# Optimization experiments

Measured on AMD Instinct MI355X. Metric: run time of the kernel, lower is better.

The kernel has to match this reference:

```python
import jax, jax.numpy as jnp
import numpy as np

B, S, E, D, A = 64, 1024, 512, 512, 512

def setup_inputs() -> dict:
    key = jax.random.key(0)
    ks = jax.random.split(key, 12)
    xavier = lambda k, shape: jax.random.uniform(k, shape, jnp.float32,
        -jnp.sqrt(6.0 / (shape[0] + shape[1])), jnp.sqrt(6.0 / (shape[0] + shape[1])))
    return {
        "encoder_states": jax.random.normal(ks[0], (B, S, E), jnp.float32),
        "decoder_state": jax.random.normal(ks[1], (B, D), jnp.float32),
        "encoder_mask": jnp.ones((B, S), jnp.int32),
        "coverage": jax.random.uniform(ks[2], (B, S), jnp.float32),
        # learned parameters (torch nn.Linear: y = x @ W.T + b)
        "W_enc": xavier(ks[3], (A, E)),           # encoder_projection, no bias
        "W_dec": xavier(ks[4], (A, D)),           # decoder_projection, no bias
        "w_attn": xavier(ks[5], (1, A)),          # attention_weight, no bias
        "W_layer1": xavier(ks[6], (A, A)),        # attention_layers[0]
        "b_layer1": jnp.zeros((A,), jnp.float32),
        "W_cov": xavier(ks[7], (A, 1)),           # coverage_projection, no bias
        "W_gate": xavier(ks[8], (A, E + D)),      # gate Linear
        "b_gate": jnp.zeros((A,), jnp.float32),
    }


def reference(encoder_states, decoder_state, encoder_mask, coverage,
              W_enc, W_dec, w_attn, W_layer1, b_layer1, W_cov, W_gate, b_gate):
    # projections
    proj_enc = jnp.einsum('bse,ae->bsa', encoder_states, W_enc)        # [B,S,A]
    proj_dec = jnp.einsum('bd,ad->ba', decoder_state, W_dec)[:, None]  # [B,1,A]
    attn_in = proj_enc + proj_dec
    # coverage: Linear(1->A) on coverage[..., None]
    attn_in = attn_in + coverage[..., None] * W_cov[None, None, :, 0]  # [B,S,A]
    feats = jnp.tanh(attn_in)
    # extra residual tanh layer (num_layers=2 -> one layer)
    feats = jnp.tanh(jnp.einsum('bsa,ca->bsc', feats, W_layer1) + b_layer1 + feats)
    scores = jnp.einsum('bsa,a->bs', feats, w_attn[0])                 # [B,S]
    scores = jnp.where(encoder_mask == 0, -1e9, scores)
    attn_w = jax.nn.softmax(scores, axis=-1)                           # [B,S]
    context = jnp.einsum('bs,bse->be', attn_w, encoder_states)         # [B,E]
    # gating
    gate_in = jnp.concatenate([context, decoder_state], axis=-1)       # [B,E+D]
    gate = jax.nn.sigmoid(jnp.einsum('bf,af->ba', gate_in, W_gate) + b_gate)
    context = gate * context
    updated_coverage = coverage + attn_w
    return (context, attn_w, updated_coverage)
```

## Files before the change

kernel.cpp:

```cpp
#include <hip/hip_runtime.h>
#include <hip/hip_bf16.h>

typedef unsigned short ushort_t;
typedef __attribute__((ext_vector_type(8))) short short8;
typedef __attribute__((ext_vector_type(4))) float float4_t;
typedef __attribute__((ext_vector_type(2))) float float2_t;
typedef __attribute__((ext_vector_type(4))) unsigned int uint4_t;

#define BB 64
#define SS 1024
#define EE 512
#define DD 512
#define AA 512
#define MM (BB*SS)
#define KK 512
#define BM 128
#define BN 128
#define BK 32
#define BKP 40
#define BK2 64
#define NT (KK/BK2)

__device__ __forceinline__ float bf2f(ushort_t u) {
    return __uint_as_float(((unsigned int)u) << 16);
}
__device__ __forceinline__ ushort_t f2bf(float f) {
    unsigned int u = __float_as_uint(f);
    unsigned int r = u + 0x7fffu + ((u >> 16) & 1u);
    return (ushort_t)(r >> 16);
}
__device__ __forceinline__ float ldmix(int f32, const void* p, long idx) {
    return f32 ? ((const float*)p)[idx] : bf2f(((const ushort_t*)p)[idx]);
}
__device__ __forceinline__ void stmix(int f32, void* p, long idx, float v) {
    if (f32) ((float*)p)[idx] = v;
    else     ((ushort_t*)p)[idx] = f2bf(v);
}
__device__ __forceinline__ float fast_tanh(float x) {
    float e = __expf(2.f * x);
    return 1.f - 2.f / (e + 1.f);
}
__device__ __forceinline__ void glds16(const ushort_t* g, ushort_t* l) {
    typedef __attribute__((address_space(1))) const void gas_t;
    typedef __attribute__((address_space(3))) void las_t;
    gas_t* gp = (gas_t*)g;
    las_t* lp = (las_t*)l;
    __builtin_amdgcn_global_load_lds(gp, lp, 16, 0, 0);
}

__global__ void k_detect(const ushort_t* __restrict__ enc, int* __restrict__ flag) {
    __shared__ int cnt;
    int tid = threadIdx.x;
    if (tid == 0) cnt = 0;
    __syncthreads();
    int c = 0;
    const uint4_t* p = (const uint4_t*)enc;
    for (int i = tid; i < 4096; i += 256) {
        uint4_t v = p[i];
        #pragma unroll
        for (int j = 0; j < 4; j++) {
            unsigned int u = v[j];
            if (((u >> 7) & 0xFFu) == 0xFFu || ((u >> 23) & 0xFFu) == 0xFFu) c++;
        }
    }
    atomicAdd(&cnt, c);
    __syncthreads();
    if (tid == 0) *flag = (cnt > 0) ? 1 : 0;
}

__global__ __launch_bounds__(256)
void k_conv_w(const void* __restrict__ Wenc, const void* __restrict__ W1,
              const int* __restrict__ flagp,
              ushort_t* __restrict__ WencB, ushort_t* __restrict__ W1B) {
    const int f32 = *flagp;
    const void* src = blockIdx.y ? W1 : Wenc;
    ushort_t* dst = blockIdx.y ? W1B : WencB;
    long e0 = ((long)blockIdx.x * 256 + threadIdx.x) * 8;
    short8 p;
    #pragma unroll
    for (int j = 0; j < 8; j++) p[j] = (short)f2bf(ldmix(f32, src, e0 + j));
    *(short8*)&dst[e0] = p;
}

__global__ __launch_bounds__(256)
void k_conv_enc(const void* __restrict__ enc, const int* __restrict__ flagp,
                ushort_t* __restrict__ out) {
    if (*flagp == 0) return;
    const float4_t* src = (const float4_t*)enc;
    size_t i0 = (size_t)blockIdx.x * 256 + threadIdx.x;
    size_t n8 = (size_t)MM * EE / 8;
    size_t stride = (size_t)gridDim.x * 256;
    for (size_t i = i0; i < n8; i += stride) {
        float4_t v0 = src[2 * i], v1 = src[2 * i + 1];
        short8 p;
        p[0] = (short)f2bf(v0[0]); p[1] = (short)f2bf(v0[1]);
        p[2] = (short)f2bf(v0[2]); p[3] = (short)f2bf(v0[3]);
        p[4] = (short)f2bf(v1[0]); p[5] = (short)f2bf(v1[1]);
        p[6] = (short)f2bf(v1[2]); p[7] = (short)f2bf(v1[3]);
        *(short8*)&out[i * 8] = p;
    }
}

__global__ __launch_bounds__(256)
void k_proj_dec(const void* __restrict__ dec,
                const void* __restrict__ Wdec,
                const int* __restrict__ flagp,
                float* __restrict__ proj) {
    __shared__ float x[DD];
    const int f32 = *flagp;
    const int b = blockIdx.y;
    const int tid = threadIdx.x, lane = tid & 63, wave = tid >> 6;
    x[tid]       = ldmix(f32, dec, (long)b * DD + tid);
    x[tid + 256] = ldmix(f32, dec, (long)b * DD + tid + 256);
    __syncthreads();
    const int a = blockIdx.x * 4 + wave;
    float s = 0.f;
    if (f32) {
        const float* wr = (const float*)Wdec + (size_t)a * DD + lane * 8;
        #pragma unroll
        for (int j = 0; j < 8; j++) s += wr[j] * x[lane * 8 + j];
    } else {
        const ushort_t* wr = (const ushort_t*)Wdec + (size_t)a * DD + lane * 8;
        short8 w = *(const short8*)wr;
        #pragma unroll
        for (int j = 0; j < 8; j++) s += bf2f((ushort_t)w[j]) * x[lane * 8 + j];
    }
    #pragma unroll
    for (int off = 1; off < 64; off <<= 1) s += __shfl_xor(s, off);
    if (lane == 0) proj[b * AA + a] = s;
}

__device__ __forceinline__ void stage8(int f32, const void* g, long row, int col,
                                       ushort_t* lds) {
    if (f32) {
        const float* gf = (const float*)g + row * KK + col;
        float4_t v0 = *(const float4_t*)(gf);
        float4_t v1 = *(const float4_t*)(gf + 4);
        short8 p;
        p[0] = (short)f2bf(v0[0]); p[1] = (short)f2bf(v0[1]);
        p[2] = (short)f2bf(v0[2]); p[3] = (short)f2bf(v0[3]);
        p[4] = (short)f2bf(v1[0]); p[5] = (short)f2bf(v1[1]);
        p[6] = (short)f2bf(v1[2]); p[7] = (short)f2bf(v1[3]);
        *(short8*)lds = p;
    } else {
        const ushort_t* gb = (const ushort_t*)g + row * KK + col;
        *(short8*)lds = *(const short8*)gb;
    }
}

__global__ __launch_bounds__(256)
void k_gemm1(const void* __restrict__ Xg,
             const void* __restrict__ Bg,
             const float* __restrict__ proj_dec,
             const void* __restrict__ cov,
             const void* __restrict__ Wcov,
             const int* __restrict__ flagp,
             ushort_t* __restrict__ feats) {
    __shared__ ushort_t As[BM * BKP];
    __shared__ ushort_t Bs[BN * BKP];
    const int f32 = *flagp;
    const int tid = threadIdx.x;
    const int lane = tid & 63, wave = tid >> 6;
    const int quad = lane >> 4, l16 = lane & 15;
    const int wm = wave >> 1, wn = wave & 1;
    const int m0 = blockIdx.y * BM, n0 = blockIdx.x * BN;

    float4_t acc[4][4];
    #pragma unroll
    for (int i = 0; i < 4; i++)
        #pragma unroll
        for (int j = 0; j < 4; j++) acc[i][j] = (float4_t){0.f, 0.f, 0.f, 0.f};

    const int srow = lane >> 2;
    const int scol = (lane & 3) * 8;
    ushort_t* lA0 = &As[(wave * 32 + srow) * BKP + scol];
    ushort_t* lB0 = &Bs[(wave * 32 + srow) * BKP + scol];

    for (int kt = 0; kt < KK; kt += BK) {
        __syncthreads();
        stage8(f32, Xg, (long)(m0 + wave * 32 + srow), kt + scol, lA0);
        stage8(f32, Xg, (long)(m0 + wave * 32 + srow + 16), kt + scol, lA0 + 16 * BKP);
        stage8(f32, Bg, (long)(n0 + wave * 32 + srow), kt + scol, lB0);
        stage8(f32, Bg, (long)(n0 + wave * 32 + srow + 16), kt + scol, lB0 + 16 * BKP);
        __syncthreads();
        short8 af[4], bfr[4];
        #pragma unroll
        for (int mt = 0; mt < 4; mt++)
            af[mt] = *(const short8*)&As[(wm * 64 + mt * 16 + l16) * BKP + quad * 8];
        #pragma unroll
        for (int nt = 0; nt < 4; nt++)
            bfr[nt] = *(const short8*)&Bs[(wn * 64 + nt * 16 + l16) * BKP + quad * 8];
        #pragma unroll
        for (int mt = 0; mt < 4; mt++)
            #pragma unroll
            for (int nt = 0; nt < 4; nt++)
                acc[mt][nt] = __builtin_amdgcn_mfma_f32_16x16x32_bf16(af[mt], bfr[nt], acc[mt][nt], 0, 0, 0);
    }

    #pragma unroll
    for (int mt = 0; mt < 4; mt++) {
        #pragma unroll
        for (int r = 0; r < 4; r++) {
            int m = m0 + wm * 64 + mt * 16 + quad * 4 + r;
            int b = m >> 10;
            float covv = ldmix(f32, cov, m);
            #pragma unroll
            for (int nt = 0; nt < 4; nt++) {
                int n = n0 + wn * 64 + nt * 16 + l16;
                float v = acc[mt][nt][r] + proj_dec[b * AA + n] + covv * ldmix(f32, Wcov, n);
                feats[(size_t)m * AA + n] = f2bf(fast_tanh(v));
            }
        }
    }
}

__global__ __launch_bounds__(256)
void k_gemm2(const ushort_t* __restrict__ Xg,
             const void* __restrict__ Bg,
             const void* __restrict__ b1,
             const void* __restrict__ wattn,
             const int* __restrict__ flagp,
             float* __restrict__ scores) {
    __shared__ ushort_t As[BM * BKP];
    __shared__ ushort_t Bs[BN * BKP];
    const int f32 = *flagp;
    const int tid = threadIdx.x;
    const int lane = tid & 63, wave = tid >> 6;
    const int quad = lane >> 4, l16 = lane & 15;
    const int wm = wave >> 1, wn = wave & 1;
    const int m0 = blockIdx.y * BM, n0 = blockIdx.x * BN;

    float4_t acc[4][4];
    #pragma unroll
    for (int i = 0; i < 4; i++)
        #pragma unroll
        for (int j = 0; j < 4; j++) acc[i][j] = (float4_t){0.f, 0.f, 0.f, 0.f};

    const int srow = lane >> 2;
    const int scol = (lane & 3) * 8;
    ushort_t* lA0 = &As[(wave * 32 + srow) * BKP + scol];
    ushort_t* lB0 = &Bs[(wave * 32 + srow) * BKP + scol];

    for (int kt = 0; kt < KK; kt += BK) {
        __syncthreads();
        stage8(0,   Xg, (long)(m0 + wave * 32 + srow), kt + scol, lA0);
        stage8(0,   Xg, (long)(m0 + wave * 32 + srow + 16), kt + scol, lA0 + 16 * BKP);
        stage8(f32, Bg, (long)(n0 + wave * 32 + srow), kt + scol, lB0);
        stage8(f32, Bg, (long)(n0 + wave * 32 + srow + 16), kt + scol, lB0 + 16 * BKP);
        __syncthreads();
        short8 af[4], bfr[4];
        #pragma unroll
        for (int mt = 0; mt < 4; mt++)
            af[mt] = *(const short8*)&As[(wm * 64 + mt * 16 + l16) * BKP + quad * 8];
        #pragma unroll
        for (int nt = 0; nt < 4; nt++)
            bfr[nt] = *(const short8*)&Bs[(wn * 64 + nt * 16 + l16) * BKP + quad * 8];
        #pragma unroll
        for (int mt = 0; mt < 4; mt++)
            #pragma unroll
            for (int nt = 0; nt < 4; nt++)
                acc[mt][nt] = __builtin_amdgcn_mfma_f32_16x16x32_bf16(af[mt], bfr[nt], acc[mt][nt], 0, 0, 0);
    }

    float wv[4], bv[4];
    #pragma unroll
    for (int nt = 0; nt < 4; nt++) {
        int n = n0 + wn * 64 + nt * 16 + l16;
        wv[nt] = ldmix(f32, wattn, n);
        bv[nt] = ldmix(f32, b1, n);
    }
    #pragma unroll
    for (int mt = 0; mt < 4; mt++) {
        #pragma unroll
        for (int r = 0; r < 4; r++) {
            int m = m0 + wm * 64 + mt * 16 + quad * 4 + r;
            float s = 0.f;
            #pragma unroll
            for (int nt = 0; nt < 4; nt++) {
                int n = n0 + wn * 64 + nt * 16 + l16;
                float v = acc[mt][nt][r] + bv[nt] + bf2f(Xg[(size_t)m * AA + n]);
                s += fast_tanh(v) * wv[nt];
            }
            s += __shfl_xor(s, 1);
            s += __shfl_xor(s, 2);
            s += __shfl_xor(s, 4);
            s += __shfl_xor(s, 8);
            if (l16 == 0) atomicAdd(&scores[m], s);
        }
    }
}

__global__ __launch_bounds__(256)
void k_gemm1n(const void* __restrict__ enc,
              const ushort_t* __restrict__ enc_bf,
              const ushort_t* __restrict__ Wenc_bf,
              const float* __restrict__ proj_dec,
              const void* __restrict__ cov,
              const void* __restrict__ Wcov,
              const int* __restrict__ flagp,
              ushort_t* __restrict__ feats) {
    __shared__ ushort_t As[BM * BK2];
    __shared__ ushort_t Bs[BN * BK2];
    const int f32 = *flagp;
    const ushort_t* Abf = f32 ? enc_bf : (const ushort_t*)enc;

    const int lid = ((blockIdx.x & 7) << 8) | (blockIdx.x >> 3);
    const int m0 = (lid >> 2) * BM;
    const int n0 = (lid & 3) * BN;

    const int tid = threadIdx.x;
    const int lane = tid & 63, wave = tid >> 6;
    const int quad = lane >> 4, l16 = lane & 15;
    const int wm = wave >> 1, wn = wave & 1;
    const int l8r = lane >> 3;
    const int l8c = ((lane & 7) ^ l8r) * 8;

    float4_t acc[4][4];
    #pragma unroll
    for (int i = 0; i < 4; i++)
        #pragma unroll
        for (int j = 0; j < 4; j++) acc[i][j] = (float4_t){0.f, 0.f, 0.f, 0.f};

    #pragma unroll
    for (int kt = 0; kt < NT; kt++) {
        __syncthreads();
        #pragma unroll
        for (int i = 0; i < 4; i++) {
            int ch = i * 4 + wave;
            glds16(Abf     + (((size_t)(m0 + ch * 8 + l8r)) << 9) + kt * BK2 + l8c, &As[ch * 512]);
            glds16(Wenc_bf + (((size_t)(n0 + ch * 8 + l8r)) << 9) + kt * BK2 + l8c, &Bs[ch * 512]);
        }
        __syncthreads();
        #pragma unroll
        for (int kk = 0; kk < 2; kk++) {
            short8 af[4], bfv[4];
            #pragma unroll
            for (int mt = 0; mt < 4; mt++) {
                int row = wm * 64 + mt * 16 + l16;
                int col = (kk * 32 + quad * 8) ^ ((row & 7) << 3);
                af[mt] = *(const short8*)&As[row * BK2 + col];
            }
            #pragma unroll
            for (int nt = 0; nt < 4; nt++) {
                int row = wn * 64 + nt * 16 + l16;
                int col = (kk * 32 + quad * 8) ^ ((row & 7) << 3);
                bfv[nt] = *(const short8*)&Bs[row * BK2 + col];
            }
            #pragma unroll
            for (int mt = 0; mt < 4; mt++)
                #pragma unroll
                for (int nt = 0; nt < 4; nt++)
                    acc[mt][nt] = __builtin_amdgcn_mfma_f32_16x16x32_bf16(af[mt], bfv[nt], acc[mt][nt], 0, 0, 0);
        }
    }

    __syncthreads();
    ushort_t* myhalf = wm ? Bs : As;
    #pragma unroll
    for (int mt = 0; mt < 4; mt++) {
        #pragma unroll
        for (int r = 0; r < 4; r++) {
            int lr = mt * 16 + quad * 4 + r;
            int grow = wm * 64 + lr;
            int m = m0 + grow;
            int b = m >> 10;
            float covv = ldmix(f32, cov, m);
            #pragma unroll
            for (int nt = 0; nt < 4; nt++) {
                int lc = wn * 64 + nt * 16 + l16;
                int n = n0 + lc;
                float v = acc[mt][nt][r] + proj_dec[b * AA + n] + covv * ldmix(f32, Wcov, n);
                myhalf[lr * 128 + (lc ^ ((grow & 7) << 3))] = f2bf(fast_tanh(v));
            }
        }
    }
    __syncthreads();
    #pragma unroll
    for (int rep = 0; rep < 8; rep++) {
        int row = rep * 16 + (tid >> 4);
        int c8 = (tid & 15) * 8;
        const ushort_t* half = (row < 64) ? As : Bs;
        short8 vv = *(const short8*)&half[(row & 63) * 128 + (c8 ^ ((row & 7) << 3))];
        *(short8*)&feats[(size_t)(m0 + row) * AA + n0 + c8] = vv;
    }
}

__global__ __launch_bounds__(256)
void k_gemm2n(const ushort_t* __restrict__ Xg,
              const ushort_t* __restrict__ W1_bf,
              const void* __restrict__ b1,
              const void* __restrict__ wattn,
              const int* __restrict__ flagp,
              float* __restrict__ scores) {
    __shared__ ushort_t As[BM * BK2];
    __shared__ ushort_t Bs[BN * BK2];
    const int f32 = *flagp;

    const int lid = ((blockIdx.x & 7) << 8) | (blockIdx.x >> 3);
    const int m0 = (lid >> 2) * BM;
    const int n0 = (lid & 3) * BN;

    const int tid = threadIdx.x;
    const int lane = tid & 63, wave = tid >> 6;
    const int quad = lane >> 4, l16 = lane & 15;
    const int wm = wave >> 1, wn = wave & 1;
    const int l8r = lane >> 3;
    const int l8c = ((lane & 7) ^ l8r) * 8;

    float4_t acc[4][4];
    #pragma unroll
    for (int i = 0; i < 4; i++)
        #pragma unroll
        for (int j = 0; j < 4; j++) acc[i][j] = (float4_t){0.f, 0.f, 0.f, 0.f};

    #pragma unroll
    for (int kt = 0; kt < NT; kt++) {
        __syncthreads();
        #pragma unroll
        for (int i = 0; i < 4; i++) {
            int ch = i * 4 + wave;
            glds16(Xg    + (((size_t)(m0 + ch * 8 + l8r)) << 9) + kt * BK2 + l8c, &As[ch * 512]);
            glds16(W1_bf + (((size_t)(n0 + ch * 8 + l8r)) << 9) + kt * BK2 + l8c, &Bs[ch * 512]);
        }
        __syncthreads();
        #pragma unroll
        for (int kk = 0; kk < 2; kk++) {
            short8 af[4], bfv[4];
            #pragma unroll
            for (int mt = 0; mt < 4; mt++) {
                int row = wm * 64 + mt * 16 + l16;
                int col = (kk * 32 + quad * 8) ^ ((row & 7) << 3);
                af[mt] = *(const short8*)&As[row * BK2 + col];
            }
            #pragma unroll
            for (int nt = 0; nt < 4; nt++) {
                int row = wn * 64 + nt * 16 + l16;
                int col = (kk * 32 + quad * 8) ^ ((row & 7) << 3);
                bfv[nt] = *(const short8*)&Bs[row * BK2 + col];
            }
            #pragma unroll
            for (int mt = 0; mt < 4; mt++)
                #pragma unroll
                for (int nt = 0; nt < 4; nt++)
                    acc[mt][nt] = __builtin_amdgcn_mfma_f32_16x16x32_bf16(af[mt], bfv[nt], acc[mt][nt], 0, 0, 0);
        }
    }

    float wv[4], bv[4];
    #pragma unroll
    for (int nt = 0; nt < 4; nt++) {
        int n = n0 + wn * 64 + nt * 16 + l16;
        wv[nt] = ldmix(f32, wattn, n);
        bv[nt] = ldmix(f32, b1, n);
    }
    #pragma unroll
    for (int mt = 0; mt < 4; mt++) {
        #pragma unroll
        for (int r = 0; r < 4; r++) {
            int m = m0 + wm * 64 + mt * 16 + quad * 4 + r;
            float s = 0.f;
            #pragma unroll
            for (int nt = 0; nt < 4; nt++) {
                int n = n0 + wn * 64 + nt * 16 + l16;
                float v = acc[mt][nt][r] + bv[nt] + bf2f(Xg[(size_t)m * AA + n]);
                s += fast_tanh(v) * wv[nt];
            }
            s += __shfl_xor(s, 1);
            s += __shfl_xor(s, 2);
            s += __shfl_xor(s, 4);
            s += __shfl_xor(s, 8);
            if (l16 == 0) atomicAdd(&scores[m], s);
        }
    }
}

__global__ void k_softmax(const float* __restrict__ scores,
                          const int* __restrict__ mask,
                          const void* __restrict__ cov,
                          const int* __restrict__ flagp,
                          float* __restrict__ attnw,
                          void* __restrict__ dout) {
    __shared__ float red[4];
    const int f32 = *flagp;
    int b = blockIdx.x, tid = threadIdx.x;
    float v[4];
    #pragma unroll
    for (int i = 0; i < 4; i++) {
        int s = tid + i * 256;
        float sc = scores[b * SS + s];
        if (mask[b * SS + s] == 0) sc = -1e9f;
        v[i] = sc;
    }
    float mx = fmaxf(fmaxf(v[0], v[1]), fmaxf(v[2], v[3]));
    #pragma unroll
    for (int off = 1; off < 64; off <<= 1) mx = fmaxf(mx, __shfl_xor(mx, off));
    if ((tid & 63) == 0) red[tid >> 6] = mx;
    __syncthreads();
    mx = fmaxf(fmaxf(red[0], red[1]), fmaxf(red[2], red[3]));
    __syncthreads();
    float e[4], sum = 0.f;
    #pragma unroll
    for (int i = 0; i < 4; i++) { e[i] = expf(v[i] - mx); sum += e[i]; }
    #pragma unroll
    for (int off = 1; off < 64; off <<= 1) sum += __shfl_xor(sum, off);
    if ((tid & 63) == 0) red[tid >> 6] = sum;
    __syncthreads();
    sum = red[0] + red[1] + red[2] + red[3];
    float inv = 1.0f / sum;
    #pragma unroll
    for (int i = 0; i < 4; i++) {
        int s = tid + i * 256;
        float w = e[i] * inv;
        attnw[b * SS + s] = w;
        stmix(f32, dout, 32768L + (long)b * SS + s, w);
        stmix(f32, dout, 98304L + (long)b * SS + s, ldmix(f32, cov, (long)b * SS + s) + w);
    }
}

__global__ void k_context_p(const void* __restrict__ enc,
                            const ushort_t* __restrict__ enc_bf,
                            const float* __restrict__ attnw,
                            const int* __restrict__ flagp,
                            float2_t* __restrict__ ctxp) {
    const int f32 = *flagp;
    const unsigned int* base = (const unsigned int*)(f32 ? (const void*)enc_bf : enc);
    int b = blockIdx.x, sc = blockIdx.y;
    int tid = threadIdx.x;
    base += ((size_t)b * SS + sc * 128) * (EE / 2);
    float a0 = 0.f, a1 = 0.f;
    const float* wrow = attnw + b * SS + sc * 128;
    for (int s = 0; s < 128; s++) {
        float w = wrow[s];
        unsigned int u = base[(size_t)s * (EE / 2) + tid];
        a0 += w * bf2f((ushort_t)(u & 0xffff));
        a1 += w * bf2f((ushort_t)(u >> 16));
    }
    ctxp[((b << 3) + sc) * 256 + tid] = (float2_t){a0, a1};
}

__global__ void k_context(const void* __restrict__ enc,
                          const ushort_t* __restrict__ enc_bf,
                          const int pre,
                          const float* __restrict__ attnw,
                          const int* __restrict__ flagp,
                          float* __restrict__ ctx) {
    int f32 = *flagp;
    const void* e = enc;
    if (pre && f32) { e = enc_bf; f32 = 0; }
    int b = blockIdx.x, sc = blockIdx.y;
    int tid = threadIdx.x;
    float a0 = 0.f, a1 = 0.f;
    const float* wrow = attnw + b * SS + sc * 128;
    if (f32) {
        const float* base = (const float*)e + ((size_t)b * SS + sc * 128) * EE;
        for (int s = 0; s < 128; s++) {
            float w = wrow[s];
            float2_t u = *(const float2_t*)(base + (size_t)s * EE + 2 * tid);
            a0 += w * u[0];
            a1 += w * u[1];
        }
    } else {
        const unsigned int* base = (const unsigned int*)e + ((size_t)b * SS + sc * 128) * (EE / 2);
        for (int s = 0; s < 128; s++) {
            float w = wrow[s];
            unsigned int u = base[(size_t)s * (EE / 2) + tid];
            a0 += w * bf2f((ushort_t)(u & 0xffff));
            a1 += w * bf2f((ushort_t)(u >> 16));
        }
    }
    atomicAdd(&ctx[b * EE + 2 * tid], a0);
    atomicAdd(&ctx[b * EE + 2 * tid + 1], a1);
}

__global__ __launch_bounds__(256)
void k_gate_p(const float2_t* __restrict__ ctxp,
              const void* __restrict__ dec,
              const void* __restrict__ Wg,
              const void* __restrict__ bg,
              const int* __restrict__ flagp,
              void* __restrict__ dout) {
    __shared__ float gin[EE + DD];
    const int f32 = *flagp;
    const int b = blockIdx.y;
    const int tid = threadIdx.x, lane = tid & 63, wave = tid >> 6;
    float c0 = 0.f, c1 = 0.f;
    #pragma unroll
    for (int sc = 0; sc < 8; sc++) {
        float2_t v = ctxp[((b << 3) + sc) * 256 + tid];
        c0 += v[0]; c1 += v[1];
    }
    gin[2 * tid] = c0;
    gin[2 * tid + 1] = c1;
    gin[EE + tid]       = ldmix(f32, dec, (long)b * DD + tid);
    gin[EE + tid + 256] = ldmix(f32, dec, (long)b * DD + tid + 256);
    __syncthreads();
    const int a = blockIdx.x * 4 + wave;
    float s = 0.f;
    if (f32) {
        const float* wr = (const float*)Wg + (size_t)a * (EE + DD) + lane * 16;
        #pragma unroll
        for (int j = 0; j < 16; j++) s += wr[j] * gin[lane * 16 + j];
    } else {
        const ushort_t* wr = (const ushort_t*)Wg + (size_t)a * (EE + DD) + lane * 16;
        short8 w0 = *(const short8*)wr;
        short8 w1 = *(const short8*)(wr + 8);
        #pragma unroll
        for (int j = 0; j < 8; j++) {
            s += bf2f((ushort_t)w0[j]) * gin[lane * 16 + j];
            s += bf2f((ushort_t)w1[j]) * gin[lane * 16 + 8 + j];
        }
    }
    #pragma unroll
    for (int off = 1; off < 64; off <<= 1) s += __shfl_xor(s, off);
    if (lane == 0) {
        float acc = s + ldmix(f32, bg, a);
        float g = 1.f / (1.f + __expf(-acc));
        stmix(f32, dout, (long)b * AA + a, g * gin[a]);
    }
}

__global__ __launch_bounds__(256)
void k_gate(const float* __restrict__ ctx,
            const void* __restrict__ dec,
            const void* __restrict__ Wg,
            const void* __restrict__ bg,
            const int* __restrict__ flagp,
            void* __restrict__ dout) {
    __shared__ float gin[EE + DD];
    const int f32 = *flagp;
    const int b = blockIdx.y;
    const int tid = threadIdx.x, lane = tid & 63, wave = tid >> 6;
    gin[2 * tid]     = ctx[b * EE + 2 * tid];
    gin[2 * tid + 1] = ctx[b * EE + 2 * tid + 1];
    gin[EE + tid]       = ldmix(f32, dec, (long)b * DD + tid);
    gin[EE + tid + 256] = ldmix(f32, dec, (long)b * DD + tid + 256);
    __syncthreads();
    const int a = blockIdx.x * 4 + wave;
    float s = 0.f;
    if (f32) {
        const float* wr = (const float*)Wg + (size_t)a * (EE + DD) + lane * 16;
        #pragma unroll
        for (int j = 0; j < 16; j++) s += wr[j] * gin[lane * 16 + j];
    } else {
        const ushort_t* wr = (const ushort_t*)Wg + (size_t)a * (EE + DD) + lane * 16;
        short8 w0 = *(const short8*)wr;
        short8 w1 = *(const short8*)(wr + 8);
        #pragma unroll
        for (int j = 0; j < 8; j++) {
            s += bf2f((ushort_t)w0[j]) * gin[lane * 16 + j];
            s += bf2f((ushort_t)w1[j]) * gin[lane * 16 + 8 + j];
        }
    }
    #pragma unroll
    for (int off = 1; off < 64; off <<= 1) s += __shfl_xor(s, off);
    if (lane == 0) {
        float acc = s + ldmix(f32, bg, a);
        float g = 1.f / (1.f + __expf(-acc));
        stmix(f32, dout, (long)b * AA + a, g * ctx[b * EE + a]);
    }
}

extern "C" void kernel_launch(void* const* d_in, const int* in_sizes, int n_in,
                              void* d_out, int out_size, void* d_ws, size_t ws_size,
                              hipStream_t stream) {
    const void* enc   = d_in[0];
    const void* dec   = d_in[1];
    const int*  mask  = (const int*)d_in[2];
    const void* cov   = d_in[3];
    const void* Wenc  = d_in[4];
    const void* Wdec  = d_in[5];
    const void* wattn = d_in[6];
    const void* Wl1   = d_in[7];
    const void* b1    = d_in[8];
    const void* Wcov  = d_in[9];
    const void* Wg    = d_in[10];
    const void* bg    = d_in[11];

    char* ws = (char*)d_ws;
    float*    scores = (float*)ws;
    float*    ctx    = (float*)(ws + 262144);
    float*    attnw  = (float*)(ws + 393216);
    float*    projd  = (float*)(ws + 655360);
    int*      flag   = (int*)(ws + 786432);
    ushort_t* feats  = (ushort_t*)(ws + 1048576);
    ushort_t* W1b    = (ushort_t*)(ws + 68157440);
    ushort_t* Wencb  = (ushort_t*)(ws + 68681728);
    ushort_t* encb   = (ushort_t*)(ws + 69206016);
    float2_t* ctxp   = (float2_t*)(ws + 136314880);
    const int pre2 = (ws_size >= 69206016UL)  ? 1 : 0;
    const int pre1 = (ws_size >= 136314880UL) ? 1 : 0;
    const int pre3 = (ws_size >= 137363456UL) ? 1 : 0;

    hipMemsetAsync(ws, 0, 393216, stream);
    k_detect<<<1, 256, 0, stream>>>((const ushort_t*)enc, flag);
    if (pre2)
        k_conv_w<<<dim3(128, 2), 256, 0, stream>>>(Wenc, Wl1, flag, Wencb, W1b);
    if (pre1)
        k_conv_enc<<<4096, 256, 0, stream>>>(enc, flag, encb);
    k_proj_dec<<<dim3(AA / 4, BB), 256, 0, stream>>>(dec, Wdec, flag, projd);
    if (pre1)
        k_gemm1n<<<2048, 256, 0, stream>>>(enc, encb, Wencb, projd, cov, Wcov, flag, feats);
    else
        k_gemm1<<<dim3(AA / BN, MM / BM), 256, 0, stream>>>(enc, Wenc, projd, cov, Wcov, flag, feats);
    if (pre2)
        k_gemm2n<<<2048, 256, 0, stream>>>(feats, W1b, b1, wattn, flag, scores);
    else
        k_gemm2<<<dim3(AA / BN, MM / BM), 256, 0, stream>>>(feats, Wl1, b1, wattn, flag, scores);
    k_softmax<<<BB, 256, 0, stream>>>(scores, mask, cov, flag, attnw, d_out);
    if (pre1 && pre3) {
        k_context_p<<<dim3(BB, 8), 256, 0, stream>>>(enc, encb, attnw, flag, ctxp);
        k_gate_p<<<dim3(AA / 4, BB), 256, 0, stream>>>(ctxp, dec, Wg, bg, flag, d_out);
    } else {
        k_context<<<dim3(BB, 8), 256, 0, stream>>>(enc, encb, pre1, attnw, flag, ctx);
        k_gate<<<dim3(AA / 4, BB), 256, 0, stream>>>(ctx, dec, Wg, bg, flag, d_out);
    }
}
```

Baseline: 399.6 us.

## Fuse prep kernels, write per-slice partial scores, infer dtype from input sizes

Merges encoder/weight bf16 conversion and decoder projection into a single prep launch. The score GEMM now writes per-column-block partial sums to separate slots, which the softmax adds up, so the atomic/memset path is no longer needed. The dtype is taken from host-side input sizes, which skips the detect kernel when the size is recognized. The new path needs a larger workspace and costs extra partial-score traffic.

```diff
diff --git a/kernel.cpp b/kernel.cpp
--- a/kernel.cpp
+++ b/kernel.cpp
@@ -40,6 +40,9 @@
     float e = __expf(2.f * x);
     return 1.f - 2.f / (e + 1.f);
 }
+__device__ __forceinline__ int getf32(const int* flagp, int fmode) {
+    return (fmode == 2) ? *flagp : fmode;
+}
 __device__ __forceinline__ void glds16(const ushort_t* g, ushort_t* l) {
     typedef __attribute__((address_space(1))) const void gas_t;
     typedef __attribute__((address_space(3))) void las_t;
@@ -69,10 +72,71 @@
 }
 
 __global__ __launch_bounds__(256)
+void k_prep(const void* __restrict__ enc, const void* __restrict__ dec,
+            const void* __restrict__ Wenc, const void* __restrict__ W1,
+            const void* __restrict__ Wdec, const int* __restrict__ flagp, const int fmode,
+            ushort_t* __restrict__ encb, ushort_t* __restrict__ WencB,
+            ushort_t* __restrict__ W1B, float* __restrict__ proj) {
+    __shared__ float x[DD];
+    const int f32 = getf32(flagp, fmode);
+    const int bx = blockIdx.x, tid = threadIdx.x;
+    if (bx < 4096) {
+        if (!f32) return;
+        const float4_t* src = (const float4_t*)enc;
+        size_t i0 = (size_t)bx * 256 + tid;
+        size_t n8 = (size_t)MM * EE / 8;
+        size_t stride = (size_t)4096 * 256;
+        for (size_t i = i0; i < n8; i += stride) {
+            float4_t v0 = src[2 * i], v1 = src[2 * i + 1];
+            short8 p;
+            p[0] = (short)f2bf(v0[0]); p[1] = (short)f2bf(v0[1]);
+            p[2] = (short)f2bf(v0[2]); p[3] = (short)f2bf(v0[3]);
+            p[4] = (short)f2bf(v1[0]); p[5] = (short)f2bf(v1[1]);
+            p[6] = (short)f2bf(v1[2]); p[7] = (short)f2bf(v1[3]);
+            *(short8*)&encb[i * 8] = p;
+        }
+        return;
+    }
+    if (bx < 4352) {
+        int idx = bx - 4096;
+        int by = idx >> 7, bxx = idx & 127;
+        const void* src = by ? W1 : Wenc;
+        ushort_t* dst = by ? W1B : WencB;
+        long e0 = ((long)bxx * 256 + tid) * 8;
+        short8 p;
+        #pragma unroll
+        for (int j = 0; j < 8; j++) p[j] = (short)f2bf(ldmix(f32, src, e0 + j));
+        *(short8*)&dst[e0] = p;
+        return;
+    }
+    int q = bx - 4352;
+    const int bxx = q & 127, b = q >> 7;
+    const int lane = tid & 63, wave = tid >> 6;
+    x[tid]       = ldmix(f32, dec, (long)b * DD + tid);
+    x[tid + 256] = ldmix(f32, dec, (long)b * DD + tid + 256);
+    __syncthreads();
+    const int a = bxx * 4 + wave;
+    float s = 0.f;
+    if (f32) {
+        const float* wr = (const float*)Wdec + (size_t)a * DD + lane * 8;
+        #pragma unroll
+        for (int j = 0; j < 8; j++) s += wr[j] * x[lane * 8 + j];
+    } else {
+        const ushort_t* wr = (const ushort_t*)Wdec + (size_t)a * DD + lane * 8;
+        short8 w = *(const short8*)wr;
+        #pragma unroll
+        for (int j = 0; j < 8; j++) s += bf2f((ushort_t)w[j]) * x[lane * 8 + j];
+    }
+    #pragma unroll
+    for (int off = 1; off < 64; off <<= 1) s += __shfl_xor(s, off);
+    if (lane == 0) proj[b * AA + a] = s;
+}
+
+__global__ __launch_bounds__(256)
 void k_conv_w(const void* __restrict__ Wenc, const void* __restrict__ W1,
-              const int* __restrict__ flagp,
+              const int* __restrict__ flagp, const int fmode,
               ushort_t* __restrict__ WencB, ushort_t* __restrict__ W1B) {
-    const int f32 = *flagp;
+    const int f32 = getf32(flagp, fmode);
     const void* src = blockIdx.y ? W1 : Wenc;
     ushort_t* dst = blockIdx.y ? W1B : WencB;
     long e0 = ((long)blockIdx.x * 256 + threadIdx.x) * 8;
@@ -83,9 +147,9 @@
 }
 
 __global__ __launch_bounds__(256)
-void k_conv_enc(const void* __restrict__ enc, const int* __restrict__ flagp,
+void k_conv_enc(const void* __restrict__ enc, const int* __restrict__ flagp, const int fmode,
                 ushort_t* __restrict__ out) {
-    if (*flagp == 0) return;
+    if (getf32(flagp, fmode) == 0) return;
     const float4_t* src = (const float4_t*)enc;
     size_t i0 = (size_t)blockIdx.x * 256 + threadIdx.x;
     size_t n8 = (size_t)MM * EE / 8;
@@ -104,10 +168,10 @@
 __global__ __launch_bounds__(256)
 void k_proj_dec(const void* __restrict__ dec,
                 const void* __restrict__ Wdec,
-                const int* __restrict__ flagp,
+                const int* __restrict__ flagp, const int fmode,
                 float* __restrict__ proj) {
     __shared__ float x[DD];
-    const int f32 = *flagp;
+    const int f32 = getf32(flagp, fmode);
     const int b = blockIdx.y;
     const int tid = threadIdx.x, lane = tid & 63, wave = tid >> 6;
     x[tid]       = ldmix(f32, dec, (long)b * DD + tid);
@@ -154,11 +218,11 @@
              const float* __restrict__ proj_dec,
              const void* __restrict__ cov,
              const void* __restrict__ Wcov,
-             const int* __restrict__ flagp,
+             const int* __restrict__ flagp, const int fmode,
              ushort_t* __restrict__ feats) {
     __shared__ ushort_t As[BM * BKP];
     __shared__ ushort_t Bs[BN * BKP];
-    const int f32 = *flagp;
+    const int f32 = getf32(flagp, fmode);
     const int tid = threadIdx.x;
     const int lane = tid & 63, wave = tid >> 6;
     const int quad = lane >> 4, l16 = lane & 15;
@@ -219,11 +283,11 @@
              const void* __restrict__ Bg,
              const void* __restrict__ b1,
              const void* __restrict__ wattn,
-             const int* __restrict__ flagp,
+             const int* __restrict__ flagp, const int fmode,
              float* __restrict__ scores) {
     __shared__ ushort_t As[BM * BKP];
     __shared__ ushort_t Bs[BN * BKP];
-    const int f32 = *flagp;
+    const int f32 = getf32(flagp, fmode);
     const int tid = threadIdx.x;
     const int lane = tid & 63, wave = tid >> 6;
     const int quad = lane >> 4, l16 = lane & 15;
@@ -297,11 +361,11 @@
               const float* __restrict__ proj_dec,
               const void* __restrict__ cov,
               const void* __restrict__ Wcov,
-              const int* __restrict__ flagp,
+              const int* __restrict__ flagp, const int fmode,
               ushort_t* __restrict__ feats) {
     __shared__ ushort_t As[BM * BK2];
     __shared__ ushort_t Bs[BN * BK2];
-    const int f32 = *flagp;
+    const int f32 = getf32(flagp, fmode);
     const ushort_t* Abf = f32 ? enc_bf : (const ushort_t*)enc;
 
     const int lid = ((blockIdx.x & 7) << 8) | (blockIdx.x >> 3);
@@ -386,19 +450,20 @@
 }
 
 __global__ __launch_bounds__(256)
-void k_gemm2n(const ushort_t* __restrict__ Xg,
+void k_gemm2p(const ushort_t* __restrict__ Xg,
               const ushort_t* __restrict__ W1_bf,
               const void* __restrict__ b1,
               const void* __restrict__ wattn,
-              const int* __restrict__ flagp,
-              float* __restrict__ scores) {
+              const int* __restrict__ flagp, const int fmode,
+              float* __restrict__ sp) {
     __shared__ ushort_t As[BM * BK2];
     __shared__ ushort_t Bs[BN * BK2];
-    const int f32 = *flagp;
+    const int f32 = getf32(flagp, fmode);
 
     const int lid = ((blockIdx.x & 7) << 8) | (blockIdx.x >> 3);
     const int m0 = (lid >> 2) * BM;
     const int n0 = (lid & 3) * BN;
+    const int nb = lid & 3;
 
     const int tid = threadIdx.x;
     const int lane = tid & 63, wave = tid >> 6;
@@ -453,6 +518,96 @@
         wv[nt] = ldmix(f32, wattn, n);
         bv[nt] = ldmix(f32, b1, n);
     }
+    const size_t slotbase = (size_t)(nb * 2 + wn) * MM;
+    #pragma unroll
+    for (int mt = 0; mt < 4; mt++) {
+        #pragma unroll
+        for (int r = 0; r < 4; r++) {
+            int m = m0 + wm * 64 + mt * 16 + quad * 4 + r;
+            float s = 0.f;
+            #pragma unroll
+            for (int nt = 0; nt < 4; nt++) {
+                int n = n0 + wn * 64 + nt * 16 + l16;
+                float v = acc[mt][nt][r] + bv[nt] + bf2f(Xg[(size_t)m * AA + n]);
+                s += fast_tanh(v) * wv[nt];
+            }
+            s += __shfl_xor(s, 1);
+            s += __shfl_xor(s, 2);
+            s += __shfl_xor(s, 4);
+            s += __shfl_xor(s, 8);
+            if (l16 == 0) sp[slotbase + m] = s;
+        }
+    }
+}
+
+__global__ __launch_bounds__(256)
+void k_gemm2n(const ushort_t* __restrict__ Xg,
+              const ushort_t* __restrict__ W1_bf,
+              const void* __restrict__ b1,
+              const void* __restrict__ wattn,
+              const int* __restrict__ flagp, const int fmode,
+              float* __restrict__ scores) {
+    __shared__ ushort_t As[BM * BK2];
+    __shared__ ushort_t Bs[BN * BK2];
+    const int f32 = getf32(flagp, fmode);
+
+    const int lid = ((blockIdx.x & 7) << 8) | (blockIdx.x >> 3);
+    const int m0 = (lid >> 2) * BM;
+    const int n0 = (lid & 3) * BN;
+
+    const int tid = threadIdx.x;
+    const int lane = tid & 63, wave = tid >> 6;
+    const int quad = lane >> 4, l16 = lane & 15;
+    const int wm = wave >> 1, wn = wave & 1;
+    const int l8r = lane >> 3;
+    const int l8c = ((lane & 7) ^ l8r) * 8;
+
+    float4_t acc[4][4];
+    #pragma unroll
+    for (int i = 0; i < 4; i++)
+        #pragma unroll
+        for (int j = 0; j < 4; j++) acc[i][j] = (float4_t){0.f, 0.f, 0.f, 0.f};
+
+    #pragma unroll
+    for (int kt = 0; kt < NT; kt++) {
+        __syncthreads();
+        #pragma unroll
+        for (int i = 0; i < 4; i++) {
+            int ch = i * 4 + wave;
+            glds16(Xg    + (((size_t)(m0 + ch * 8 + l8r)) << 9) + kt * BK2 + l8c, &As[ch * 512]);
+            glds16(W1_bf + (((size_t)(n0 + ch * 8 + l8r)) << 9) + kt * BK2 + l8c, &Bs[ch * 512]);
+        }
+        __syncthreads();
+        #pragma unroll
+        for (int kk = 0; kk < 2; kk++) {
+            short8 af[4], bfv[4];
+            #pragma unroll
+            for (int mt = 0; mt < 4; mt++) {
+                int row = wm * 64 + mt * 16 + l16;
+                int col = (kk * 32 + quad * 8) ^ ((row & 7) << 3);
+                af[mt] = *(const short8*)&As[row * BK2 + col];
+            }
+            #pragma unroll
+            for (int nt = 0; nt < 4; nt++) {
+                int row = wn * 64 + nt * 16 + l16;
+                int col = (kk * 32 + quad * 8) ^ ((row & 7) << 3);
+                bfv[nt] = *(const short8*)&Bs[row * BK2 + col];
+            }
+            #pragma unroll
+            for (int mt = 0; mt < 4; mt++)
+                #pragma unroll
+                for (int nt = 0; nt < 4; nt++)
+                    acc[mt][nt] = __builtin_amdgcn_mfma_f32_16x16x32_bf16(af[mt], bfv[nt], acc[mt][nt], 0, 0, 0);
+        }
+    }
+
+    float wv[4], bv[4];
+    #pragma unroll
+    for (int nt = 0; nt < 4; nt++) {
+        int n = n0 + wn * 64 + nt * 16 + l16;
+        wv[nt] = ldmix(f32, wattn, n);
+        bv[nt] = ldmix(f32, b1, n);
+    }
     #pragma unroll
     for (int mt = 0; mt < 4; mt++) {
         #pragma unroll
@@ -474,20 +629,22 @@
     }
 }
 
-__global__ void k_softmax(const float* __restrict__ scores,
-                          const int* __restrict__ mask,
-                          const void* __restrict__ cov,
-                          const int* __restrict__ flagp,
-                          float* __restrict__ attnw,
-                          void* __restrict__ dout) {
+__global__ void k_softmax_p(const float* __restrict__ sp,
+                            const int* __restrict__ mask,
+                            const void* __restrict__ cov,
+                            const int* __restrict__ flagp, const int fmode,
+                            float* __restrict__ attnw,
+                            void* __restrict__ dout) {
     __shared__ float red[4];
-    const int f32 = *flagp;
+    const int f32 = getf32(flagp, fmode);
     int b = blockIdx.x, tid = threadIdx.x;
     float v[4];
     #pragma unroll
     for (int i = 0; i < 4; i++) {
         int s = tid + i * 256;
-        float sc = scores[b * SS + s];
+        float sc = 0.f;
+        #pragma unroll
+        for (int k = 0; k < 8; k++) sc += sp[(size_t)k * MM + b * SS + s];
         if (mask[b * SS + s] == 0) sc = -1e9f;
         v[i] = sc;
     }
@@ -517,12 +674,55 @@
     }
 }
 
+__global__ void k_softmax(const float* __restrict__ scores,
+                          const int* __restrict__ mask,
+                          const void* __restrict__ cov,
+                          const int* __restrict__ flagp, const int fmode,
+                          float* __restrict__ attnw,
+                          void* __restrict__ dout) {
+    __shared__ float red[4];
+    const int f32 = getf32(flagp, fmode);
+    int b = blockIdx.x, tid = threadIdx.x;
+    float v[4];
+    #pragma unroll
+    for (int i = 0; i < 4; i++) {
+        int s = tid + i * 256;
+        float sc = scores[b * SS + s];
+        if (mask[b * SS + s] == 0) sc = -1e9f;
+        v[i] = sc;
+    }
+    float mx = fmaxf(fmaxf(v[0], v[1]), fmaxf(v[2], v[3]));
+    #pragma unroll
+    for (int off = 1; off < 64; off <<= 1) mx = fmaxf(mx, __shfl_xor(mx, off));
+    if ((tid & 63) == 0) red[tid >> 6] = mx;
+    __syncthreads();
+    mx = fmaxf(fmaxf(red[0], red[1]), fmaxf(red[2], red[3]));
+    __syncthreads();
+    float e[4], sum = 0.f;
+    #pragma unroll
+    for (int i = 0; i < 4; i++) { e[i] = expf(v[i] - mx); sum += e[i]; }
+    #pragma unroll
+    for (int off = 1; off < 64; off <<= 1) sum += __shfl_xor(sum, off);
+    if ((tid & 63) == 0) red[tid >> 6] = sum;
+    __syncthreads();
+    sum = red[0] + red[1] + red[2] + red[3];
+    float inv = 1.0f / sum;
+    #pragma unroll
+    for (int i = 0; i < 4; i++) {
+        int s = tid + i * 256;
+        float w = e[i] * inv;
+        attnw[b * SS + s] = w;
+        stmix(f32, dout, 32768L + (long)b * SS + s, w);
+        stmix(f32, dout, 98304L + (long)b * SS + s, ldmix(f32, cov, (long)b * SS + s) + w);
+    }
+}
+
 __global__ void k_context_p(const void* __restrict__ enc,
                             const ushort_t* __restrict__ enc_bf,
                             const float* __restrict__ attnw,
-                            const int* __restrict__ flagp,
+                            const int* __restrict__ flagp, const int fmode,
                             float2_t* __restrict__ ctxp) {
-    const int f32 = *flagp;
+    const int f32 = getf32(flagp, fmode);
     const unsigned int* base = (const unsigned int*)(f32 ? (const void*)enc_bf : enc);
     int b = blockIdx.x, sc = blockIdx.y;
     int tid = threadIdx.x;
@@ -542,9 +742,9 @@
                           const ushort_t* __restrict__ enc_bf,
                           const int pre,
                           const float* __restrict__ attnw,
-                          const int* __restrict__ flagp,
+                          const int* __restrict__ flagp, const int fmode,
                           float* __restrict__ ctx) {
-    int f32 = *flagp;
+    int f32 = getf32(flagp, fmode);
     const void* e = enc;
     if (pre && f32) { e = enc_bf; f32 = 0; }
     int b = blockIdx.x, sc = blockIdx.y;
@@ -577,10 +777,10 @@
               const void* __restrict__ dec,
               const void* __restrict__ Wg,
               const void* __restrict__ bg,
-              const int* __restrict__ flagp,
+              const int* __restrict__ flagp, const int fmode,
               void* __restrict__ dout) {
     __shared__ float gin[EE + DD];
-    const int f32 = *flagp;
+    const int f32 = getf32(flagp, fmode);
     const int b = blockIdx.y;
     const int tid = threadIdx.x, lane = tid & 63, wave = tid >> 6;
     float c0 = 0.f, c1 = 0.f;
@@ -624,10 +824,10 @@
             const void* __restrict__ dec,
             const void* __restrict__ Wg,
             const void* __restrict__ bg,
-            const int* __restrict__ flagp,
+            const int* __restrict__ flagp, const int fmode,
             void* __restrict__ dout) {
     __shared__ float gin[EE + DD];
-    const int f32 = *flagp;
+    const int f32 = getf32(flagp, fmode);
     const int b = blockIdx.y;
     const int tid = threadIdx.x, lane = tid & 63, wave = tid >> 6;
     gin[2 * tid]     = ctx[b * EE + 2 * tid];
@@ -687,31 +887,55 @@
     ushort_t* Wencb  = (ushort_t*)(ws + 68681728);
     ushort_t* encb   = (ushort_t*)(ws + 69206016);
     float2_t* ctxp   = (float2_t*)(ws + 136314880);
+    float*    sp     = (float*)(ws + 137363456);
+
+    int fmode = 2;
+    if (in_sizes && n_in > 0) {
+        if (in_sizes[0] == 134217728) fmode = 1;
+        else if (in_sizes[0] == 67108864) fmode = 0;
+    }
+
+    const int full = (ws_size >= 139460608UL) ? 1 : 0;
+
+    if (full) {
+        if (fmode == 2)
+            k_detect<<<1, 256, 0, stream>>>((const ushort_t*)enc, flag);
+        k_prep<<<12544, 256, 0, stream>>>(enc, dec, Wenc, Wl1, Wdec, flag, fmode,
+                                          encb, Wencb, W1b, projd);
+        k_gemm1n<<<2048, 256, 0, stream>>>(enc, encb, Wencb, projd, cov, Wcov, flag, fmode, feats);
+        k_gemm2p<<<2048, 256, 0, stream>>>(feats, W1b, b1, wattn, flag, fmode, sp);
+        k_softmax_p<<<BB, 256, 0, stream>>>(sp, mask, cov, flag, fmode, attnw, d_out);
+        k_context_p<<<dim3(BB, 8), 256, 0, stream>>>(enc, encb, attnw, flag, fmode, ctxp);
+        k_gate_p<<<dim3(AA / 4, BB), 256, 0, stream>>>(ctxp, dec, Wg, bg, flag, fmode, d_out);
+        return;
+    }
+
     const int pre2 = (ws_size >= 69206016UL)  ? 1 : 0;
     const int pre1 = (ws_size >= 136314880UL) ? 1 : 0;
     const int pre3 = (ws_size >= 137363456UL) ? 1 : 0;
 
     hipMemsetAsync(ws, 0, 393216, stream);
-    k_detect<<<1, 256, 0, stream>>>((const ushort_t*)enc, flag);
+    if (fmode == 2)
+        k_detect<<<1, 256, 0, stream>>>((const ushort_t*)enc, flag);
     if (pre2)
-        k_conv_w<<<dim3(128, 2), 256, 0, stream>>>(Wenc, Wl1, flag, Wencb, W1b);
+        k_conv_w<<<dim3(128, 2), 256, 0, stream>>>(Wenc, Wl1, flag, fmode, Wencb, W1b);
     if (pre1)
-        k_conv_enc<<<4096, 256, 0, stream>>>(enc, flag, encb);
-    k_proj_dec<<<dim3(AA / 4, BB), 256, 0, stream>>>(dec, Wdec, flag, projd);
+        k_conv_enc<<<4096, 256, 0, stream>>>(enc, flag, fmode, encb);
+    k_proj_dec<<<dim3(AA / 4, BB), 256, 0, stream>>>(dec, Wdec, flag, fmode, projd);
     if (pre1)
-        k_gemm1n<<<2048, 256, 0, stream>>>(enc, encb, Wencb, projd, cov, Wcov, flag, feats);
+        k_gemm1n<<<2048, 256, 0, stream>>>(enc, encb, Wencb, projd, cov, Wcov, flag, fmode, feats);
     else
-        k_gemm1<<<dim3(AA / BN, MM / BM), 256, 0, stream>>>(enc, Wenc, projd, cov, Wcov, flag, feats);
+        k_gemm1<<<dim3(AA / BN, MM / BM), 256, 0, stream>>>(enc, Wenc, projd, cov, Wcov, flag, fmode, feats);
     if (pre2)
-        k_gemm2n<<<2048, 256, 0, stream>>>(feats, W1b, b1, wattn, flag, scores);
+        k_gemm2n<<<2048, 256, 0, stream>>>(feats, W1b, b1, wattn, flag, fmode, scores);
     else
-        k_gemm2<<<dim3(AA / BN, MM / BM), 256, 0, stream>>>(feats, Wl1, b1, wattn, flag, scores);
-    k_softmax<<<BB, 256, 0, stream>>>(scores, mask, cov, flag, attnw, d_out);
+        k_gemm2<<<dim3(AA / BN, MM / BM), 256, 0, stream>>>(feats, Wl1, b1, wattn, flag, fmode, scores);
+    k_softmax<<<BB, 256, 0, stream>>>(scores, mask, cov, flag, fmode, attnw, d_out);
     if (pre1 && pre3) {
-        k_context_p<<<dim3(BB, 8), 256, 0, stream>>>(enc, encb, attnw, flag, ctxp);
-        k_gate_p<<<dim3(AA / 4, BB), 256, 0, stream>>>(ctxp, dec, Wg, bg, flag, d_out);
+        k_context_p<<<dim3(BB, 8), 256, 0, stream>>>(enc, encb, attnw, flag, fmode, ctxp);
+        k_gate_p<<<dim3(AA / 4, BB), 256, 0, stream>>>(ctxp, dec, Wg, bg, flag, fmode, d_out);
     } else {
-        k_context<<<dim3(BB, 8), 256, 0, stream>>>(enc, encb, pre1, attnw, flag, ctx);
-        k_gate<<<dim3(AA / 4, BB), 256, 0, stream>>>(ctx, dec, Wg, bg, flag, d_out);
-    }
-}
+        k_context<<<dim3(BB, 8), 256, 0, stream>>>(enc, encb, pre1, attnw, flag, fmode, ctx);
+        k_gate<<<dim3(AA / 4, BB), 256, 0, stream>>>(ctx, dec, Wg, bg, flag, fmode, d_out);
+    }
+}
```

Result: no change. 400.5 us (+0.2%).
